# Performance work log

Measured on AMD Instinct MI355X. Metric: run time of the kernel, lower is better.

Reference implementation:

```python
import jax, jax.numpy as jnp
import numpy as np

NUM_EMBEDDINGS = 1024
EMBEDDING_DIM = 256
COMMITMENT_COST = 0.25


def setup_inputs() -> dict:
    key = jax.random.key(0)
    kz, kc = jax.random.split(key)
    z = jax.random.normal(kz, (32, 32, 32, EMBEDDING_DIM), dtype=jnp.float32)
    # torch init: uniform(-1/K, 1/K)
    codebook = jax.random.uniform(
        kc, (NUM_EMBEDDINGS, EMBEDDING_DIM), dtype=jnp.float32,
        minval=-1.0 / NUM_EMBEDDINGS, maxval=1.0 / NUM_EMBEDDINGS)
    return {"z": z, "codebook": codebook}


def reference(z, codebook):
    K, D = codebook.shape
    zf = z.reshape(-1, D)                                   # [N, D]
    # squared L2 distances via expansion: ||z||^2 + ||e||^2 - 2 z.e
    distances = (jnp.sum(zf * zf, axis=1, keepdims=True)
                 + jnp.sum(codebook * codebook, axis=1)
                 - 2.0 * jnp.matmul(zf, codebook.T))        # [N, K]
    idx = jnp.argmin(distances, axis=1)                     # [N]
    encodings = jax.nn.one_hot(idx, K, dtype=z.dtype)       # [N, K]
    quantized = jnp.matmul(encodings, codebook).reshape(z.shape)
    e_latent_loss = jnp.mean((jax.lax.stop_gradient(quantized) - z) ** 2)
    q_latent_loss = jnp.mean((quantized - jax.lax.stop_gradient(z)) ** 2)
    loss = q_latent_loss + COMMITMENT_COST * e_latent_loss
    quantized_st = z + jax.lax.stop_gradient(quantized - z)  # straight-through
    return quantized_st, loss, encodings
```

## Files before the change

kernel.cpp:

```cpp
#include <hip/hip_runtime.h>

#define N_ROWS 32768
#define DIM 256
#define K_CODES 1024
#define OUT_QUANT 8388608

typedef unsigned long long ull;
typedef __attribute__((ext_vector_type(8))) short bf16x8;
typedef __attribute__((ext_vector_type(4))) float f32x4;

__device__ __forceinline__ float pw128sq(const float* __restrict__ x) {
  float r[8];
#pragma unroll
  for (int j = 0; j < 8; ++j) r[j] = __fmul_rn(x[j], x[j]);
#pragma unroll
  for (int i = 8; i < 128; i += 8) {
#pragma unroll
    for (int j = 0; j < 8; ++j) r[j] = __fadd_rn(r[j], __fmul_rn(x[i + j], x[i + j]));
  }
  return __fadd_rn(__fadd_rn(__fadd_rn(r[0], r[1]), __fadd_rn(r[2], r[3])),
                   __fadd_rn(__fadd_rn(r[4], r[5]), __fadd_rn(r[6], r[7])));
}

__global__ __launch_bounds__(256) void row_norms(const float* __restrict__ z,
                                                 float* __restrict__ rn) {
  int r = blockIdx.x * 256 + threadIdx.x;
  if (r < N_ROWS)
    rn[r] = __fadd_rn(pw128sq(z + (size_t)r * DIM), pw128sq(z + (size_t)r * DIM + 128));
}

__global__ __launch_bounds__(256) void code_norms(const float* __restrict__ cb,
                                                  float* __restrict__ cn) {
  int k = blockIdx.x * 256 + threadIdx.x;
  if (k < K_CODES)
    cn[k] = __fadd_rn(pw128sq(cb + (size_t)k * DIM), pw128sq(cb + (size_t)k * DIM + 128));
}

__device__ __forceinline__ void split3(float x, unsigned short& h, unsigned short& m,
                                       unsigned short& l) {
  unsigned int u = __float_as_uint(x);
  unsigned int hb = u & 0xFFFF0000u;
  h = (unsigned short)(hb >> 16);
  float r1 = __fsub_rn(x, __uint_as_float(hb));
  unsigned int mb = __float_as_uint(r1) & 0xFFFF0000u;
  m = (unsigned short)(mb >> 16);
  float r2 = __fsub_rn(r1, __uint_as_float(mb));
  unsigned int u2 = __float_as_uint(r2);
  unsigned int rounded = u2 + 0x7FFFu + ((u2 >> 16) & 1u);
  l = (unsigned short)(rounded >> 16);
}

__global__ __launch_bounds__(256) void split_z(const float* __restrict__ z,
                                               unsigned short* __restrict__ zh,
                                               unsigned short* __restrict__ zm,
                                               unsigned short* __restrict__ zl) {
  const size_t i = ((size_t)blockIdx.x * 256 + threadIdx.x) * 4;
  const float4 v = *(const float4*)(z + i);
  ushort4 h, m, l;
  split3(v.x, h.x, m.x, l.x);
  split3(v.y, h.y, m.y, l.y);
  split3(v.z, h.z, m.z, l.z);
  split3(v.w, h.w, m.w, l.w);
  *(ushort4*)(zh + i) = h;
  *(ushort4*)(zm + i) = m;
  *(ushort4*)(zl + i) = l;
}

__device__ __forceinline__ void lds16(const void* g, void* l) {
  __builtin_amdgcn_global_load_lds(
      (const __attribute__((address_space(1))) unsigned int*)g,
      (__attribute__((address_space(3))) unsigned int*)l, 16, 0, 0);
}

__device__ __forceinline__ ull shflx64(ull v, int m) {
  int lo = __shfl_xor((int)(v & 0xffffffffull), m);
  int hi = __shfl_xor((int)(v >> 32), m);
  return ((ull)(unsigned int)hi << 32) | (unsigned int)lo;
}

__global__ __launch_bounds__(256) void gemm_argmin_mfma(
    const unsigned short* __restrict__ zh, const unsigned short* __restrict__ zm,
    const unsigned short* __restrict__ zl, const unsigned short* __restrict__ ch,
    const unsigned short* __restrict__ cm, const unsigned short* __restrict__ cl,
    const float* __restrict__ rn, const float* __restrict__ cn,
    ull* __restrict__ keys) {
  __shared__ unsigned short As[4 * 128 * 8];
  __shared__ unsigned short Bs[4 * 128 * 8];

  const int bid = blockIdx.x;
  const int xcd = bid & 7;
  const int i = bid >> 3;
  const int bm = xcd * 32 + (i >> 3);
  const int bn = i & 7;
  const int row0 = bm * 128, col0 = bn * 128;

  const int tid = threadIdx.x;
  const int wid = tid >> 6, lane = tid & 63;
  const int wm = wid >> 1, wn = wid & 1;
  const int lq = lane >> 4, lr = lane & 15;
  const int srow = tid & 127, shalf = tid >> 7;

  f32x4 acc[4][4];
#pragma unroll
  for (int a = 0; a < 4; ++a)
#pragma unroll
    for (int b = 0; b < 4; ++b) acc[a][b] = (f32x4){0.f, 0.f, 0.f, 0.f};

  const unsigned short* As_g_row = nullptr;

  auto kpass = [&](const unsigned short* __restrict__ Ag,
                   const unsigned short* __restrict__ Bg) {
    for (int kk = 0; kk < DIM; kk += 32) {
      __syncthreads();
#pragma unroll
      for (int is = 0; is < 2; ++is) {
        lds16(Ag + (size_t)(row0 + srow) * DIM + kk + is * 16 + shalf * 8,
              (char*)As + is * 4096 + tid * 16);
        lds16(Bg + (size_t)(col0 + srow) * DIM + kk + is * 16 + shalf * 8,
              (char*)Bs + is * 4096 + tid * 16);
      }
      __syncthreads();

      bf16x8 av[4], bv[4];
      const bf16x8* As8 = (const bf16x8*)As;
      const bf16x8* Bs8 = (const bf16x8*)Bs;
#pragma unroll
      for (int fm = 0; fm < 4; ++fm) av[fm] = As8[lq * 128 + wm * 64 + fm * 16 + lr];
#pragma unroll
      for (int fn = 0; fn < 4; ++fn) bv[fn] = Bs8[lq * 128 + wn * 64 + fn * 16 + lr];
#pragma unroll
      for (int fm = 0; fm < 4; ++fm)
#pragma unroll
        for (int fn = 0; fn < 4; ++fn)
          acc[fm][fn] = __builtin_amdgcn_mfma_f32_16x16x32_bf16(av[fm], bv[fn],
                                                                acc[fm][fn], 0, 0, 0);
    }
  };

  kpass(zh, ch);
  kpass(zh, cm);
  kpass(zm, ch);
  kpass(zh, cl);
  kpass(zl, ch);
  kpass(zm, cm);
  (void)As_g_row;

  float cnv[4];
#pragma unroll
  for (int fn = 0; fn < 4; ++fn) cnv[fn] = cn[col0 + wn * 64 + fn * 16 + lr];

#pragma unroll
  for (int fm = 0; fm < 4; ++fm) {
#pragma unroll
    for (int j = 0; j < 4; ++j) {
      const int rg = row0 + wm * 64 + fm * 16 + lq * 4 + j;
      const float a_rn = rn[rg];
      ull best = ~0ull;
#pragma unroll
      for (int fn = 0; fn < 4; ++fn) {
        const int cg = col0 + wn * 64 + fn * 16 + lr;
        const float d = __fsub_rn(__fadd_rn(a_rn, cnv[fn]), 2.0f * acc[fm][fn][j]);
        unsigned int b = __float_as_uint(d);
        b = (b & 0x80000000u) ? ~b : (b | 0x80000000u);
        const ull key = ((ull)b << 32) | (unsigned int)cg;
        if (key < best) best = key;
      }
#pragma unroll
      for (int off = 1; off <= 8; off <<= 1) {
        ull o = shflx64(best, off);
        if (o < best) best = o;
      }
      if (lr == 0) atomicMin(&keys[rg], best);
    }
  }
}

__global__ __launch_bounds__(256) void quantize_out(
    const float* __restrict__ z, const float* __restrict__ cb,
    const ull* __restrict__ keys, float* __restrict__ out,
    float* __restrict__ lossp) {
  __shared__ float ls[4];
  const int wid = threadIdx.x >> 6, lane = threadIdx.x & 63;
  const int row = blockIdx.x * 4 + wid;
  const int idx = (int)(keys[row] & 0xffffffffull);
  const float4 zv = *(const float4*)(z + (size_t)row * DIM + lane * 4);
  const float4 qv = *(const float4*)(cb + (size_t)idx * DIM + lane * 4);
  const float dx = __fsub_rn(qv.x, zv.x);
  const float dy = __fsub_rn(qv.y, zv.y);
  const float dzz = __fsub_rn(qv.z, zv.z);
  const float dw = __fsub_rn(qv.w, zv.w);
  float4 ov;
  ov.x = __fadd_rn(zv.x, dx); ov.y = __fadd_rn(zv.y, dy);
  ov.z = __fadd_rn(zv.z, dzz); ov.w = __fadd_rn(zv.w, dw);
  *(float4*)(out + (size_t)row * DIM + lane * 4) = ov;
  float s = dx * dx + dy * dy + dzz * dzz + dw * dw;
#pragma unroll
  for (int o = 32; o > 0; o >>= 1) s += __shfl_down(s, o);
  if (lane == 0) ls[wid] = s;

  float4* enc4 = (float4*)(out + (size_t)OUT_QUANT + 1 + (size_t)row * K_CODES);
  const int target = idx >> 2, comp = idx & 3;
#pragma unroll
  for (int i = 0; i < 4; ++i) {
    const int f4i = lane + 64 * i;
    float4 v = {0.f, 0.f, 0.f, 0.f};
    if (f4i == target) ((float*)&v)[comp] = 1.0f;
    enc4[f4i] = v;
  }

  __syncthreads();
  if (threadIdx.x == 0) lossp[blockIdx.x] = ls[0] + ls[1] + ls[2] + ls[3];
}

__global__ __launch_bounds__(256) void loss_final(const float* __restrict__ lossp,
                                                  float* __restrict__ out) {
  __shared__ float sm[256];
  float v = 0.f;
  for (int i = threadIdx.x; i < 8192; i += 256) v += lossp[i];
  sm[threadIdx.x] = v;
  __syncthreads();
  for (int s = 128; s > 0; s >>= 1) {
    if (threadIdx.x < s) sm[threadIdx.x] += sm[threadIdx.x + s];
    __syncthreads();
  }
  if (threadIdx.x == 0) out[OUT_QUANT] = sm[0] * (1.25f / 8388608.0f);
}

extern "C" void kernel_launch(void* const* d_in, const int* in_sizes, int n_in,
                              void* d_out, int out_size, void* d_ws, size_t ws_size,
                              hipStream_t stream) {
  const float* z = (const float*)d_in[0];
  const float* cb = (const float*)d_in[1];
  float* out = (float*)d_out;

  char* w = (char*)d_ws;
  ull* keys = (ull*)w;
  float* rn = (float*)(w + (256u << 10));
  float* cn = (float*)(w + (384u << 10));
  float* lossp = (float*)(w + (388u << 10));
  unsigned short* zh = (unsigned short*)(w + (1u << 20));
  unsigned short* zm = (unsigned short*)(w + (17u << 20));
  unsigned short* zl = (unsigned short*)(w + (33u << 20));
  unsigned short* ch = (unsigned short*)(w + (49u << 20));
  unsigned short* cm = (unsigned short*)(w + (49u << 20) + (512u << 10));
  unsigned short* cl = (unsigned short*)(w + (50u << 20));

  hipMemsetAsync(keys, 0xFF, (size_t)N_ROWS * 8, stream);

  row_norms<<<N_ROWS / 256, 256, 0, stream>>>(z, rn);
  code_norms<<<K_CODES / 256, 256, 0, stream>>>(cb, cn);
  split_z<<<(N_ROWS * DIM) / 1024, 256, 0, stream>>>(z, zh, zm, zl);
  split_z<<<(K_CODES * DIM) / 1024, 256, 0, stream>>>(cb, ch, cm, cl);
  gemm_argmin_mfma<<<2048, 256, 0, stream>>>(zh, zm, zl, ch, cm, cl, rn, cn, keys);
  quantize_out<<<N_ROWS / 4, 256, 0, stream>>>(z, cb, keys, out, lossp);
  loss_final<<<1, 256, 0, stream>>>(lossp, out);
}
```

Baseline: 472.3 us.

## Replace 6-pass bf16 split GEMM with 3-term fp16 split and fused prep

Replaces the three-way bf16 split (six GEMM passes over K=256) with a two-way fp16 hi/lo split. The codebook is prescaled by 1024 and the lo term by 4096, and the three product terms are concatenated into one K=768 GEMM with an accumulator rescale partway through. The GEMM mainloop becomes double-buffered with one barrier per step. Norms, splits, key init and loss zeroing are merged into a single prep kernel, and the loss reduction moves to atomicAdd, removing the memset and two launches. The risk is precision: fp16 range and subnormal flushing could change argmin ties relative to the fp32 reference.

```diff
diff --git a/kernel.cpp b/kernel.cpp
--- a/kernel.cpp
+++ b/kernel.cpp
@@ -3,67 +3,92 @@
 #define N_ROWS 32768
 #define DIM 256
 #define K_CODES 1024
+#define KTOT 768
 #define OUT_QUANT 8388608
 
 typedef unsigned long long ull;
-typedef __attribute__((ext_vector_type(8))) short bf16x8;
+typedef _Float16 f16;
+typedef __attribute__((ext_vector_type(4))) _Float16 f16x4;
+typedef __attribute__((ext_vector_type(8))) _Float16 f16x8;
 typedef __attribute__((ext_vector_type(4))) float f32x4;
 
-__device__ __forceinline__ float pw128sq(const float* __restrict__ x) {
-  float r[8];
-#pragma unroll
-  for (int j = 0; j < 8; ++j) r[j] = __fmul_rn(x[j], x[j]);
-#pragma unroll
-  for (int i = 8; i < 128; i += 8) {
-#pragma unroll
-    for (int j = 0; j < 8; ++j) r[j] = __fadd_rn(r[j], __fmul_rn(x[i + j], x[i + j]));
-  }
-  return __fadd_rn(__fadd_rn(__fadd_rn(r[0], r[1]), __fadd_rn(r[2], r[3])),
-                   __fadd_rn(__fadd_rn(r[4], r[5]), __fadd_rn(r[6], r[7])));
-}
-
-__global__ __launch_bounds__(256) void row_norms(const float* __restrict__ z,
-                                                 float* __restrict__ rn) {
-  int r = blockIdx.x * 256 + threadIdx.x;
-  if (r < N_ROWS)
-    rn[r] = __fadd_rn(pw128sq(z + (size_t)r * DIM), pw128sq(z + (size_t)r * DIM + 128));
-}
-
-__global__ __launch_bounds__(256) void code_norms(const float* __restrict__ cb,
-                                                  float* __restrict__ cn) {
-  int k = blockIdx.x * 256 + threadIdx.x;
-  if (k < K_CODES)
-    cn[k] = __fadd_rn(pw128sq(cb + (size_t)k * DIM), pw128sq(cb + (size_t)k * DIM + 128));
-}
-
-__device__ __forceinline__ void split3(float x, unsigned short& h, unsigned short& m,
-                                       unsigned short& l) {
-  unsigned int u = __float_as_uint(x);
-  unsigned int hb = u & 0xFFFF0000u;
-  h = (unsigned short)(hb >> 16);
-  float r1 = __fsub_rn(x, __uint_as_float(hb));
-  unsigned int mb = __float_as_uint(r1) & 0xFFFF0000u;
-  m = (unsigned short)(mb >> 16);
-  float r2 = __fsub_rn(r1, __uint_as_float(mb));
-  unsigned int u2 = __float_as_uint(r2);
-  unsigned int rounded = u2 + 0x7FFFu + ((u2 >> 16) & 1u);
-  l = (unsigned short)(rounded >> 16);
-}
-
-__global__ __launch_bounds__(256) void split_z(const float* __restrict__ z,
-                                               unsigned short* __restrict__ zh,
-                                               unsigned short* __restrict__ zm,
-                                               unsigned short* __restrict__ zl) {
-  const size_t i = ((size_t)blockIdx.x * 256 + threadIdx.x) * 4;
-  const float4 v = *(const float4*)(z + i);
-  ushort4 h, m, l;
-  split3(v.x, h.x, m.x, l.x);
-  split3(v.y, h.y, m.y, l.y);
-  split3(v.z, h.z, m.z, l.z);
-  split3(v.w, h.w, m.w, l.w);
-  *(ushort4*)(zh + i) = h;
-  *(ushort4*)(zm + i) = m;
-  *(ushort4*)(zl + i) = l;
+#define NB_ZSPLIT 8192
+#define NB_ZNORM 2048
+#define NB_CSPLIT 256
+#define NB_CNORM 64
+
+struct HL { f16 h, l; };
+__device__ __forceinline__ HL split2(float x) {
+  f16 hh = (f16)x;
+  if (__builtin_fabsf(x) < 6.103515625e-05f) hh = (f16)0.0f;
+  const float r = __fsub_rn(x, (float)hh);
+  HL o;
+  o.h = hh;
+  o.l = (f16)(__fmul_rn(r, 4096.0f));
+  return o;
+}
+
+__global__ __launch_bounds__(256) void prep(
+    const float* __restrict__ z, const float* __restrict__ cb,
+    f16* __restrict__ Ap, f16* __restrict__ Bp,
+    float* __restrict__ rn, float* __restrict__ cn,
+    ull* __restrict__ keys, float* __restrict__ out) {
+  const int b = blockIdx.x, tid = threadIdx.x;
+  if (b < NB_ZSPLIT) {
+    const size_t g = ((size_t)b * 256 + tid) * 4;
+    const int row = (int)(g >> 8), k = (int)(g & 255);
+    const float4 v = *(const float4*)(z + g);
+    const HL s0 = split2(v.x), s1 = split2(v.y), s2 = split2(v.z), s3 = split2(v.w);
+    const f16x4 h = {s0.h, s1.h, s2.h, s3.h};
+    const f16x4 l = {s0.l, s1.l, s2.l, s3.l};
+    f16* arow = Ap + (size_t)row * KTOT + k;
+    *(f16x4*)(arow) = h;
+    *(f16x4*)(arow + 256) = l;
+    *(f16x4*)(arow + 512) = h;
+  } else if (b < NB_ZSPLIT + NB_ZNORM) {
+    const int row = (b - NB_ZSPLIT) * 16 + (tid >> 4);
+    const int j = tid & 7, half = (tid >> 3) & 1;
+    const float* x = z + (size_t)row * DIM + half * 128 + j;
+    float r = __fmul_rn(x[0], x[0]);
+#pragma unroll
+    for (int t = 1; t < 16; ++t) r = __fadd_rn(r, __fmul_rn(x[8 * t], x[8 * t]));
+    r = __fadd_rn(r, __shfl_xor(r, 1));
+    r = __fadd_rn(r, __shfl_xor(r, 2));
+    r = __fadd_rn(r, __shfl_xor(r, 4));
+    const float o = __shfl_xor(r, 8);
+    if ((tid & 15) == 0) {
+      rn[row] = __fadd_rn(r, o);
+      keys[row] = ~0ull;
+    }
+  } else if (b < NB_ZSPLIT + NB_ZNORM + NB_CSPLIT) {
+    const int b2 = b - (NB_ZSPLIT + NB_ZNORM);
+    const size_t g = ((size_t)b2 * 256 + tid) * 4;
+    const int row = (int)(g >> 8), k = (int)(g & 255);
+    const float4 v = *(const float4*)(cb + g);
+    const HL s0 = split2(__fmul_rn(v.x, 1024.0f));
+    const HL s1 = split2(__fmul_rn(v.y, 1024.0f));
+    const HL s2 = split2(__fmul_rn(v.z, 1024.0f));
+    const HL s3 = split2(__fmul_rn(v.w, 1024.0f));
+    const f16x4 h = {s0.h, s1.h, s2.h, s3.h};
+    const f16x4 l = {s0.l, s1.l, s2.l, s3.l};
+    f16* brow = Bp + (size_t)row * KTOT + k;
+    *(f16x4*)(brow) = h;
+    *(f16x4*)(brow + 256) = h;
+    *(f16x4*)(brow + 512) = l;
+    if (b2 == 0 && tid == 0) out[OUT_QUANT] = 0.0f;
+  } else {
+    const int row = (b - (NB_ZSPLIT + NB_ZNORM + NB_CSPLIT)) * 16 + (tid >> 4);
+    const int j = tid & 7, half = (tid >> 3) & 1;
+    const float* x = cb + (size_t)row * DIM + half * 128 + j;
+    float r = __fmul_rn(x[0], x[0]);
+#pragma unroll
+    for (int t = 1; t < 16; ++t) r = __fadd_rn(r, __fmul_rn(x[8 * t], x[8 * t]));
+    r = __fadd_rn(r, __shfl_xor(r, 1));
+    r = __fadd_rn(r, __shfl_xor(r, 2));
+    r = __fadd_rn(r, __shfl_xor(r, 4));
+    const float o = __shfl_xor(r, 8);
+    if ((tid & 15) == 0) cn[row] = __fadd_rn(r, o);
+  }
 }
 
 __device__ __forceinline__ void lds16(const void* g, void* l) {
@@ -78,72 +103,68 @@
   return ((ull)(unsigned int)hi << 32) | (unsigned int)lo;
 }
 
-__global__ __launch_bounds__(256) void gemm_argmin_mfma(
-    const unsigned short* __restrict__ zh, const unsigned short* __restrict__ zm,
-    const unsigned short* __restrict__ zl, const unsigned short* __restrict__ ch,
-    const unsigned short* __restrict__ cm, const unsigned short* __restrict__ cl,
+__global__ __launch_bounds__(256) void gemm_argmin_f16(
+    const f16* __restrict__ Ap, const f16* __restrict__ Bp,
     const float* __restrict__ rn, const float* __restrict__ cn,
     ull* __restrict__ keys) {
-  __shared__ unsigned short As[4 * 128 * 8];
-  __shared__ unsigned short Bs[4 * 128 * 8];
+  __shared__ f16 As[2][4096];
+  __shared__ f16 Bs[2][4096];
 
   const int bid = blockIdx.x;
-  const int xcd = bid & 7;
-  const int i = bid >> 3;
-  const int bm = xcd * 32 + (i >> 3);
-  const int bn = i & 7;
+  const int xcd = bid & 7, ii = bid >> 3;
+  const int bm = xcd * 32 + (ii >> 3), bn = ii & 7;
   const int row0 = bm * 128, col0 = bn * 128;
-
-  const int tid = threadIdx.x;
-  const int wid = tid >> 6, lane = tid & 63;
-  const int wm = wid >> 1, wn = wid & 1;
-  const int lq = lane >> 4, lr = lane & 15;
+  const int tid = threadIdx.x, wid = tid >> 6, lane = tid & 63;
+  const int wm = wid >> 1, wn = wid & 1, lq = lane >> 4, lr = lane & 15;
   const int srow = tid & 127, shalf = tid >> 7;
 
   f32x4 acc[4][4];
 #pragma unroll
   for (int a = 0; a < 4; ++a)
 #pragma unroll
-    for (int b = 0; b < 4; ++b) acc[a][b] = (f32x4){0.f, 0.f, 0.f, 0.f};
-
-  const unsigned short* As_g_row = nullptr;
-
-  auto kpass = [&](const unsigned short* __restrict__ Ag,
-                   const unsigned short* __restrict__ Bg) {
-    for (int kk = 0; kk < DIM; kk += 32) {
-      __syncthreads();
+    for (int c = 0; c < 4; ++c) acc[a][c] = (f32x4){0.f, 0.f, 0.f, 0.f};
+
+  const f16* aG = Ap + (size_t)(row0 + srow) * KTOT + shalf * 8;
+  const f16* bG = Bp + (size_t)(col0 + srow) * KTOT + shalf * 8;
+
+#pragma unroll
+  for (int is = 0; is < 2; ++is) {
+    lds16(aG + is * 16, (char*)As[0] + is * 4096 + tid * 16);
+    lds16(bG + is * 16, (char*)Bs[0] + is * 4096 + tid * 16);
+  }
+  __syncthreads();
+
+#pragma unroll
+  for (int t = 0; t < 24; ++t) {
+    const int cur = t & 1, nxt = cur ^ 1;
+    if (t < 23) {
 #pragma unroll
       for (int is = 0; is < 2; ++is) {
-        lds16(Ag + (size_t)(row0 + srow) * DIM + kk + is * 16 + shalf * 8,
-              (char*)As + is * 4096 + tid * 16);
-        lds16(Bg + (size_t)(col0 + srow) * DIM + kk + is * 16 + shalf * 8,
-              (char*)Bs + is * 4096 + tid * 16);
+        lds16(aG + (t + 1) * 32 + is * 16, (char*)As[nxt] + is * 4096 + tid * 16);
+        lds16(bG + (t + 1) * 32 + is * 16, (char*)Bs[nxt] + is * 4096 + tid * 16);
       }
-      __syncthreads();
-
-      bf16x8 av[4], bv[4];
-      const bf16x8* As8 = (const bf16x8*)As;
-      const bf16x8* Bs8 = (const bf16x8*)Bs;
-#pragma unroll
-      for (int fm = 0; fm < 4; ++fm) av[fm] = As8[lq * 128 + wm * 64 + fm * 16 + lr];
-#pragma unroll
-      for (int fn = 0; fn < 4; ++fn) bv[fn] = Bs8[lq * 128 + wn * 64 + fn * 16 + lr];
-#pragma unroll
-      for (int fm = 0; fm < 4; ++fm)
-#pragma unroll
-        for (int fn = 0; fn < 4; ++fn)
-          acc[fm][fn] = __builtin_amdgcn_mfma_f32_16x16x32_bf16(av[fm], bv[fn],
-                                                                acc[fm][fn], 0, 0, 0);
-    }
-  };
-
-  kpass(zh, ch);
-  kpass(zh, cm);
-  kpass(zm, ch);
-  kpass(zh, cl);
-  kpass(zl, ch);
-  kpass(zm, cm);
-  (void)As_g_row;
+    }
+    if (t == 8) {
+#pragma unroll
+      for (int a = 0; a < 4; ++a)
+#pragma unroll
+        for (int c = 0; c < 4; ++c) acc[a][c] *= 4096.0f;
+    }
+    f16x8 av[4], bv[4];
+    const f16x8* As8 = (const f16x8*)As[cur];
+    const f16x8* Bs8 = (const f16x8*)Bs[cur];
+#pragma unroll
+    for (int fm = 0; fm < 4; ++fm) av[fm] = As8[lq * 128 + wm * 64 + fm * 16 + lr];
+#pragma unroll
+    for (int fn = 0; fn < 4; ++fn) bv[fn] = Bs8[lq * 128 + wn * 64 + fn * 16 + lr];
+#pragma unroll
+    for (int fm = 0; fm < 4; ++fm)
+#pragma unroll
+      for (int fn = 0; fn < 4; ++fn)
+        acc[fm][fn] = __builtin_amdgcn_mfma_f32_16x16x32_f16(av[fm], bv[fn],
+                                                             acc[fm][fn], 0, 0, 0);
+    __syncthreads();
+  }
 
   float cnv[4];
 #pragma unroll
@@ -159,10 +180,11 @@
 #pragma unroll
       for (int fn = 0; fn < 4; ++fn) {
         const int cg = col0 + wn * 64 + fn * 16 + lr;
-        const float d = __fsub_rn(__fadd_rn(a_rn, cnv[fn]), 2.0f * acc[fm][fn][j]);
-        unsigned int b = __float_as_uint(d);
-        b = (b & 0x80000000u) ? ~b : (b | 0x80000000u);
-        const ull key = ((ull)b << 32) | (unsigned int)cg;
+        const float d = __fsub_rn(__fadd_rn(a_rn, cnv[fn]),
+                                  __fmul_rn(acc[fm][fn][j], 4.76837158203125e-07f));
+        unsigned int mono = __float_as_uint(d);
+        mono = (mono & 0x80000000u) ? ~mono : (mono | 0x80000000u);
+        const ull key = ((ull)mono << 32) | (unsigned int)cg;
         if (key < best) best = key;
       }
 #pragma unroll
@@ -177,8 +199,7 @@
 
 __global__ __launch_bounds__(256) void quantize_out(
     const float* __restrict__ z, const float* __restrict__ cb,
-    const ull* __restrict__ keys, float* __restrict__ out,
-    float* __restrict__ lossp) {
+    const ull* __restrict__ keys, float* __restrict__ out) {
   __shared__ float ls[4];
   const int wid = threadIdx.x >> 6, lane = threadIdx.x & 63;
   const int row = blockIdx.x * 4 + wid;
@@ -209,21 +230,8 @@
   }
 
   __syncthreads();
-  if (threadIdx.x == 0) lossp[blockIdx.x] = ls[0] + ls[1] + ls[2] + ls[3];
-}
-
-__global__ __launch_bounds__(256) void loss_final(const float* __restrict__ lossp,
-                                                  float* __restrict__ out) {
-  __shared__ float sm[256];
-  float v = 0.f;
-  for (int i = threadIdx.x; i < 8192; i += 256) v += lossp[i];
-  sm[threadIdx.x] = v;
-  __syncthreads();
-  for (int s = 128; s > 0; s >>= 1) {
-    if (threadIdx.x < s) sm[threadIdx.x] += sm[threadIdx.x + s];
-    __syncthreads();
-  }
-  if (threadIdx.x == 0) out[OUT_QUANT] = sm[0] * (1.25f / 8388608.0f);
+  if (threadIdx.x == 0)
+    atomicAdd(out + OUT_QUANT, (ls[0] + ls[1] + ls[2] + ls[3]) * (1.25f / 8388608.0f));
 }
 
 extern "C" void kernel_launch(void* const* d_in, const int* in_sizes, int n_in,
@@ -237,21 +245,11 @@
   ull* keys = (ull*)w;
   float* rn = (float*)(w + (256u << 10));
   float* cn = (float*)(w + (384u << 10));
-  float* lossp = (float*)(w + (388u << 10));
-  unsigned short* zh = (unsigned short*)(w + (1u << 20));
-  unsigned short* zm = (unsigned short*)(w + (17u << 20));
-  unsigned short* zl = (unsigned short*)(w + (33u << 20));
-  unsigned short* ch = (unsigned short*)(w + (49u << 20));
-  unsigned short* cm = (unsigned short*)(w + (49u << 20) + (512u << 10));
-  unsigned short* cl = (unsigned short*)(w + (50u << 20));
-
-  hipMemsetAsync(keys, 0xFF, (size_t)N_ROWS * 8, stream);
-
-  row_norms<<<N_ROWS / 256, 256, 0, stream>>>(z, rn);
-  code_norms<<<K_CODES / 256, 256, 0, stream>>>(cb, cn);
-  split_z<<<(N_ROWS * DIM) / 1024, 256, 0, stream>>>(z, zh, zm, zl);
-  split_z<<<(K_CODES * DIM) / 1024, 256, 0, stream>>>(cb, ch, cm, cl);
-  gemm_argmin_mfma<<<2048, 256, 0, stream>>>(zh, zm, zl, ch, cm, cl, rn, cn, keys);
-  quantize_out<<<N_ROWS / 4, 256, 0, stream>>>(z, cb, keys, out, lossp);
-  loss_final<<<1, 256, 0, stream>>>(lossp, out);
-}
+  f16* Ap = (f16*)(w + (512u << 10));
+  f16* Bp = (f16*)(w + (512u << 10) + (48u << 20));
+
+  prep<<<NB_ZSPLIT + NB_ZNORM + NB_CSPLIT + NB_CNORM, 256, 0, stream>>>(
+      z, cb, Ap, Bp, rn, cn, keys, out);
+  gemm_argmin_f16<<<2048, 256, 0, stream>>>(Ap, Bp, rn, cn, keys);
+  quantize_out<<<N_ROWS / 4, 256, 0, stream>>>(z, cb, keys, out);
+}
```

New measurement: 439.2 us. 7.0% less time.
